# Optimization experiments

Measured on AMD Instinct MI355X. Metric: run time of the kernel, lower is better.

Reference implementation:

```python
import jax, jax.numpy as jnp
import numpy as np

B, H, W = 8, 448, 448
NUM_CLASSES, NUM_FEATURES = 80, 1280
TOPN, THRESHOLD = 4, 0.5


def conv(x, w, b, stride, pad):
    y = jax.lax.conv_general_dilated(x, w, (stride, stride), [(pad, pad), (pad, pad)],
                                     dimension_numbers=('NCHW', 'OIHW', 'NCHW'))
    return y + b[None, :, None, None]


def sample_bilinear(img, ys, xs):
    # img: [C, Hs, Ws]; ys: [oh] float coords; xs: [ow] float coords (align_corners=True grid)
    Hs, Ws = img.shape[1], img.shape[2]
    y0 = jnp.clip(jnp.floor(ys), 0.0, Hs - 1.0)
    x0 = jnp.clip(jnp.floor(xs), 0.0, Ws - 1.0)
    y0i = y0.astype(jnp.int32); y1i = jnp.minimum(y0i + 1, Hs - 1)
    x0i = x0.astype(jnp.int32); x1i = jnp.minimum(x0i + 1, Ws - 1)
    wy = (ys - y0)[:, None]   # [oh,1]
    wx = (xs - x0)[None, :]   # [1,ow]
    r0 = img[:, y0i, :]; r1 = img[:, y1i, :]          # [C,oh,Ws]
    a = r0[:, :, x0i]; b_ = r0[:, :, x1i]             # [C,oh,ow]
    c = r1[:, :, x0i]; d = r1[:, :, x1i]
    top = a * (1.0 - wx) + b_ * wx
    bot = c * (1.0 - wx) + d * wx
    return top * (1.0 - wy) + bot * wy


def minmax_norm(s):
    # torch: if max==min: s/max else (s-min)/(max-min); sigmoid output so max>0
    mn = s.min(-1, keepdims=True); mx = s.max(-1, keepdims=True)
    rng = mx - mn
    return jnp.where(rng > 0, (s - mn) / jnp.where(rng > 0, rng, 1.0),
                     s / jnp.where(mx != 0, mx, 1.0))


def obj_loc(score, threshold, dim):
    # first/last threshold crossing with min-size fallback (vectorized over leading dims)
    mask = score >= threshold
    any_ = mask.any(-1)
    first = jnp.argmax(mask, axis=-1)
    last = dim - jnp.argmax(mask[..., ::-1], axis=-1)   # exclusive
    lo = jnp.where(any_, first, int(dim * 0.125)).astype(jnp.int32)
    hi = jnp.where(any_, last, int(dim * 0.875)).astype(jnp.int32)
    minsize = int(np.ceil(dim * 0.125))
    need = jnp.maximum(minsize - (hi - lo), 0)
    lo = jnp.maximum(lo - (need + 1) // 2, 0)
    hi = jnp.minimum(hi + (need + 1) // 2, dim)
    return lo, hi


def one_crop(img, y1, y2, x1, x2):
    # crop img[:, y1:y2, x1:x2] and bilinearly resize to (H,W), align_corners=True
    oh, ow = img.shape[1], img.shape[2]
    ys = y1.astype(jnp.float32) + jnp.arange(oh, dtype=jnp.float32) * ((y2 - 1 - y1).astype(jnp.float32) / (oh - 1))
    xs = x1.astype(jnp.float32) + jnp.arange(ow, dtype=jnp.float32) * ((x2 - 1 - x1).astype(jnp.float32) / (ow - 1))
    return sample_bilinear(img, ys, xs)


def setup_inputs() -> dict:
    key = jax.random.key(0)
    k1, k2, k3 = jax.random.split(key, 3)
    return {
        'inputs': jax.random.normal(k1, (B, 3, H, W), dtype=jnp.float32),
        'feat_w': jax.random.normal(k2, (NUM_FEATURES, 3, 3, 3), dtype=jnp.float32) * 0.05,
        'feat_b': jnp.zeros((NUM_FEATURES,), dtype=jnp.float32),
        'cls_w': jax.random.normal(k3, (NUM_CLASSES, NUM_FEATURES, 1, 1), dtype=jnp.float32) * 0.02,
        'cls_b': jnp.zeros((NUM_CLASSES,), dtype=jnp.float32),
    }


def reference(inputs, feat_w, feat_b, cls_w, cls_b):
    b, c, h, w = inputs.shape
    # ---- backbone (stride-32 stand-in for MobileNetV2 features) ----
    ga = jnp.clip(conv(inputs, feat_w, feat_b, 32, 1), 0.0, 6.0)     # [b,1280,h/32,w/32]
    gf = ga.mean((2, 3), keepdims=True)                               # avg pool sh=h/32
    gs = jax.nn.sigmoid(conv(gf, cls_w, cls_b, 1, 0)).reshape(b, -1)  # [b,num_classes]
    # ---- CAM score path (on detached ga) ----
    cam = jax.nn.sigmoid(conv(jax.lax.stop_gradient(ga), cls_w, cls_b, 1, 0))
    ys_g = jnp.linspace(0.0, cam.shape[2] - 1.0, h)
    xs_g = jnp.linspace(0.0, cam.shape[3] - 1.0, w)
    cam_up = jax.vmap(lambda im: sample_bilinear(im, ys_g, xs_g))(cam)  # [b,C,h,w]
    wscore = cam_up.max(axis=2)   # max over height -> [b,C,w]
    hscore = cam_up.max(axis=3)   # max over width  -> [b,C,h]
    # ---- topN classes by global score ----
    _, topi = jax.lax.top_k(gs, TOPN)                                  # [b,topN]
    xs_s = jnp.take_along_axis(wscore, topi[:, :, None], axis=1)       # [b,topN,w]
    ys_s = jnp.take_along_axis(hscore, topi[:, :, None], axis=1)       # [b,topN,h]
    x1, x2 = obj_loc(minmax_norm(xs_s), THRESHOLD, w)
    y1, y2 = obj_loc(minmax_norm(ys_s), THRESHOLD, h)
    # ---- dynamic crop + bilinear resize, vectorized over (b, topN) ----
    crops = jax.vmap(lambda img, a1, a2, b1, b2:
                     jax.vmap(lambda p, q, r, s: one_crop(img, p, q, r, s))(a1, a2, b1, b2)
                     )(inputs, y1, y2, x1, x2)                          # [b,topN,3,h,w]
    li = jax.lax.stop_gradient(crops.reshape(b * TOPN, 3, h, w))
    la = jnp.clip(conv(li, feat_w, feat_b, 32, 1), 0.0, 6.0)
    lf = la.mean((2, 3), keepdims=True)
    ls = jax.nn.sigmoid(conv(lf, cls_w, cls_b, 1, 0)).reshape(b, TOPN, -1).max(axis=1)
    return gs, ls
```

## Files before the change

### kernel.cpp

```cpp
#include <hip/hip_runtime.h>
#include <math.h>

#define NB 8
#define TOPN 4
#define NC 80
#define NF 1280
#define HW 448
#define OS 14
#define NP 196
#define NPCH 49
#define PATCH (3*42*42)

__device__ __forceinline__ float sigmoidf_(float x) { return 1.0f / (1.0f + expf(-x)); }

__device__ __forceinline__ double wave_reduce_f64(double v) {
#pragma unroll
  for (int off = 32; off > 0; off >>= 1) v += __shfl_down(v, off);
  return v;
}

__global__ __launch_bounds__(256) void k1_conv_global(
    const float* __restrict__ in,
    const float* __restrict__ fw,
    const float* __restrict__ fb,
    float* __restrict__ ga,
    double* __restrict__ gfp)
{
  __shared__ float patch[PATCH];
  const int b = blockIdx.y, fc = blockIdx.x, pz = blockIdx.z, tid = threadIdx.x;
  for (int i = tid; i < PATCH; i += 256) {
    int c = i / 1764, rem = i % 1764, r = rem / 42, cc = rem % 42;
    int row = 32 * (r / 3) + (r % 3) - 1;
    int col = 32 * (cc / 3) + (cc % 3) - 1;
    float v = 0.0f;
    if (row >= 0 && col >= 0)
      v = in[((b * 3 + c) * HW + row) * HW + col];
    patch[i] = v;
  }
  __syncthreads();
  const int f = fc * 256 + tid;
  float w[27];
#pragma unroll
  for (int k = 0; k < 27; ++k) w[k] = fw[f * 27 + k];
  const float bias = fb[f];
  double sum = 0.0;
#pragma unroll 7
  for (int pi = 0; pi < NPCH; ++pi) {
    const int p = pz * NPCH + pi;
    const int oy = p / OS, ox = p % OS;
    float acc = bias;
#pragma unroll
    for (int c = 0; c < 3; ++c)
#pragma unroll
      for (int ky = 0; ky < 3; ++ky)
#pragma unroll
        for (int kx = 0; kx < 3; ++kx)
          acc += patch[c * 1764 + (oy * 3 + ky) * 42 + (ox * 3 + kx)] * w[c * 9 + ky * 3 + kx];
    acc = fminf(fmaxf(acc, 0.0f), 6.0f);
    ga[((size_t)b * NP + p) * NF + f] = acc;
    sum += (double)acc;
  }
  gfp[((size_t)pz * NB + b) * NF + f] = sum;
}

__global__ __launch_bounds__(64) void k2a_gs(
    const double* __restrict__ gfp,
    const float* __restrict__ cw,
    const float* __restrict__ cb,
    float* __restrict__ gs_out)
{
  const int cls = blockIdx.x, b = blockIdx.y, lane = threadIdx.x;
  const float* w = cw + (size_t)cls * NF;
  const double* g0 = gfp + ((size_t)0 * NB + b) * NF;
  const double* g1 = gfp + ((size_t)1 * NB + b) * NF;
  const double* g2 = gfp + ((size_t)2 * NB + b) * NF;
  const double* g3 = gfp + ((size_t)3 * NB + b) * NF;
  double acc = 0.0;
#pragma unroll
  for (int k = 0; k < NF / 64; ++k) {
    const int f = k * 64 + lane;
    const double gv = (double)(float)((g0[f] + g1[f] + g2[f] + g3[f]) / 196.0);
    acc += (double)w[f] * gv;
  }
  acc = wave_reduce_f64(acc);
  if (lane == 0) gs_out[b * NC + cls] = sigmoidf_((float)(acc + (double)cb[cls]));
}

__global__ __launch_bounds__(64) void k2b_topk(
    const float* __restrict__ gs,
    int* __restrict__ topi)
{
  const int b = blockIdx.x, lane = threadIdx.x;
  float v0 = gs[b * NC + lane];
  float v1 = (lane < NC - 64) ? gs[b * NC + 64 + lane] : -1e30f;
  const int i0 = lane, i1 = 64 + lane;
#pragma unroll
  for (int t = 0; t < TOPN; ++t) {
    float bv; int bi;
    if (v1 > v0) { bv = v1; bi = i1; } else { bv = v0; bi = i0; }
#pragma unroll
    for (int off = 1; off < 64; off <<= 1) {
      float ov = __shfl_xor(bv, off);
      int oi = __shfl_xor(bi, off);
      if (ov > bv || (ov == bv && oi < bi)) { bv = ov; bi = oi; }
    }
    if (lane == 0) topi[b * TOPN + t] = bi;
    if (bi == i0) v0 = -1e30f;
    if (bi == i1) v1 = -1e30f;
  }
}

__global__ __launch_bounds__(256) void k3a_cam(
    const float* __restrict__ ga,
    const float* __restrict__ cw,
    const float* __restrict__ cb,
    const int* __restrict__ topi,
    float* __restrict__ camg)
{
  const int pc = blockIdx.x, bt = blockIdx.y;
  const int tid = threadIdx.x, wid = tid >> 6, lane = tid & 63;
  const int p = pc * 4 + wid;
  const int b = bt >> 2;
  const int cls = topi[bt];
  const float* w = cw + (size_t)cls * NF;
  const float* g = ga + ((size_t)b * NP + p) * NF;
  double acc = 0.0;
#pragma unroll
  for (int k = 0; k < NF / 64; ++k) {
    const int f = k * 64 + lane;
    acc += (double)g[f] * (double)w[f];
  }
  acc = wave_reduce_f64(acc);
  if (lane == 0) camg[bt * NP + p] = sigmoidf_((float)(acc + (double)cb[cls]));
}

__global__ __launch_bounds__(256) void k3b_bounds_stage(
    const float* __restrict__ camg,
    const float* __restrict__ in,
    float* __restrict__ patchg)
{
  __shared__ float cam[NP];
  __shared__ float wsS[HW];
  __shared__ float hsS[HW];
  __shared__ int jlo[OS], jhi[OS];
  __shared__ int shb[4];
  const int bt = blockIdx.x, tid = threadIdx.x;
  const int wid = tid >> 6, lane = tid & 63;
  const float SC = 13.0f / 447.0f;

  if (tid < OS) { jlo[tid] = 1 << 30; jhi[tid] = -1; }
  for (int i = tid; i < NP; i += 256) cam[i] = camg[bt * NP + i];
  __syncthreads();
  for (int j = tid; j < HW; j += 256) {
    float yp = (float)j * SC;
    int y0 = (int)floorf(yp); if (y0 > 13) y0 = 13;
    atomicMin(&jlo[y0], j);
    atomicMax(&jhi[y0], j);
  }
  __syncthreads();

  for (int x = tid; x < HW; x += 256) {
    float xp = (float)x * SC;
    int x0 = (int)floorf(xp); if (x0 > 13) x0 = 13;
    float wx = xp - (float)x0;
    int x1i = min(x0 + 1, 13);
    {
      float cv[OS];
#pragma unroll
      for (int r = 0; r < OS; ++r)
        cv[r] = cam[r * OS + x0] * (1.0f - wx) + cam[r * OS + x1i] * wx;
      float m = -1e30f;
#pragma unroll
      for (int r = 0; r < OS; ++r) {
        int jl = jlo[r], jh = jhi[r];
        if (jl <= jh) {
          const int rn = (r + 1 < OS) ? r + 1 : OS - 1;
          float yp1 = (float)jl * SC; float wy1 = yp1 - (float)r;
          float yp2 = (float)jh * SC; float wy2 = yp2 - (float)r;
          float v1 = cv[r] * (1.0f - wy1) + cv[rn] * wy1;
          float v2 = cv[r] * (1.0f - wy2) + cv[rn] * wy2;
          m = fmaxf(m, fmaxf(v1, v2));
        }
      }
      wsS[x] = m;
    }
    {
      float cv[OS];
#pragma unroll
      for (int c = 0; c < OS; ++c)
        cv[c] = cam[x0 * OS + c] * (1.0f - wx) + cam[x1i * OS + c] * wx;
      float m = -1e30f;
#pragma unroll
      for (int r = 0; r < OS; ++r) {
        int jl = jlo[r], jh = jhi[r];
        if (jl <= jh) {
          const int rn = (r + 1 < OS) ? r + 1 : OS - 1;
          float xp1 = (float)jl * SC; float w1 = xp1 - (float)r;
          float xp2 = (float)jh * SC; float w2 = xp2 - (float)r;
          float v1 = cv[r] * (1.0f - w1) + cv[rn] * w1;
          float v2 = cv[r] * (1.0f - w2) + cv[rn] * w2;
          m = fmaxf(m, fmaxf(v1, v2));
        }
      }
      hsS[x] = m;
    }
  }
  __syncthreads();

  if (wid < 2) {
    const float* s = (wid == 0) ? wsS : hsS;
    float v[7];
    float mn = 1e30f, mx = -1e30f;
#pragma unroll
    for (int q = 0; q < 7; ++q) {
      v[q] = s[lane + 64 * q];
      mn = fminf(mn, v[q]); mx = fmaxf(mx, v[q]);
    }
#pragma unroll
    for (int off = 32; off > 0; off >>= 1) {
      mn = fminf(mn, __shfl_down(mn, off));
      mx = fmaxf(mx, __shfl_down(mx, off));
    }
    mn = __shfl(mn, 0); mx = __shfl(mx, 0);
    float rng = mx - mn;
    float dnm = (mx != 0.0f) ? mx : 1.0f;
    int firstL = 1 << 30, lastL = -1;
#pragma unroll
    for (int q = 0; q < 7; ++q) {
      float nv = (rng > 0.0f) ? (v[q] - mn) / rng : v[q] / dnm;
      if (nv >= 0.5f) {
        int idx = lane + 64 * q;
        firstL = min(firstL, idx);
        lastL = max(lastL, idx);
      }
    }
#pragma unroll
    for (int off = 32; off > 0; off >>= 1) {
      firstL = min(firstL, __shfl_down(firstL, off));
      lastL = max(lastL, __shfl_down(lastL, off));
    }
    if (lane == 0) {
      int lo, hi;
      if (lastL >= 0) { lo = firstL; hi = lastL + 1; }
      else { lo = 56; hi = 392; }
      int need = 56 - (hi - lo); if (need < 0) need = 0;
      int pad = (need + 1) >> 1;
      lo = lo - pad; if (lo < 0) lo = 0;
      hi = hi + pad; if (hi > HW) hi = HW;
      if (wid == 0) { shb[2] = lo; shb[3] = hi; }
      else          { shb[0] = lo; shb[1] = hi; }
    }
  }
  __syncthreads();

  const int b = bt >> 2;
  const int y1 = shb[0], y2 = shb[1], x1 = shb[2], x2 = shb[3];
  const float y1f = (float)y1, x1f = (float)x1;
  const float sy = (float)(y2 - 1 - y1) / 447.0f;
  const float sx = (float)(x2 - 1 - x1) / 447.0f;
  const float* img = in + (size_t)b * 3 * HW * HW;
  for (int i = tid; i < PATCH; i += 256) {
    int c = i / 1764, rem = i % 1764, r = rem / 42, cc = rem % 42;
    int yy = 32 * (r / 3) + (r % 3) - 1;
    int xx = 32 * (cc / 3) + (cc % 3) - 1;
    float v = 0.0f;
    if (yy >= 0 && xx >= 0) {
      float ys = y1f + (float)yy * sy;
      float xs = x1f + (float)xx * sx;
      float y0 = floorf(ys); if (y0 < 0.0f) y0 = 0.0f; if (y0 > 447.0f) y0 = 447.0f;
      float x0 = floorf(xs); if (x0 < 0.0f) x0 = 0.0f; if (x0 > 447.0f) x0 = 447.0f;
      int y0i = (int)y0, x0i = (int)x0;
      int y1i = min(y0i + 1, HW - 1), x1i = min(x0i + 1, HW - 1);
      float wy = ys - y0, wx = xs - x0;
      const float* ic = img + (size_t)c * HW * HW;
      float a  = ic[y0i * HW + x0i], bb = ic[y0i * HW + x1i];
      float cc2 = ic[y1i * HW + x0i], d  = ic[y1i * HW + x1i];
      float top = a * (1.0f - wx) + bb * wx;
      float bot = cc2 * (1.0f - wx) + d * wx;
      v = top * (1.0f - wy) + bot * wy;
    }
    patchg[(size_t)bt * PATCH + i] = v;
  }
}

__global__ __launch_bounds__(256) void k4_conv_local(
    const float* __restrict__ patchg,
    const float* __restrict__ fw,
    const float* __restrict__ fb,
    double* __restrict__ lfp)
{
  __shared__ float patch[PATCH];
  const int bt = blockIdx.y, fc = blockIdx.x, pz = blockIdx.z, tid = threadIdx.x;
  for (int i = tid; i < PATCH; i += 256)
    patch[i] = patchg[(size_t)bt * PATCH + i];
  __syncthreads();
  const int f = fc * 256 + tid;
  float w[27];
#pragma unroll
  for (int k = 0; k < 27; ++k) w[k] = fw[f * 27 + k];
  const float bias = fb[f];
  double sum = 0.0;
#pragma unroll 7
  for (int pi = 0; pi < NPCH; ++pi) {
    const int p = pz * NPCH + pi;
    const int oy = p / OS, ox = p % OS;
    float acc = bias;
#pragma unroll
    for (int c = 0; c < 3; ++c)
#pragma unroll
      for (int ky = 0; ky < 3; ++ky)
#pragma unroll
        for (int kx = 0; kx < 3; ++kx)
          acc += patch[c * 1764 + (oy * 3 + ky) * 42 + (ox * 3 + kx)] * w[c * 9 + ky * 3 + kx];
    acc = fminf(fmaxf(acc, 0.0f), 6.0f);
    sum += (double)acc;
  }
  lfp[((size_t)pz * (NB * TOPN) + bt) * NF + f] = sum;
}

__global__ __launch_bounds__(256) void kcomb_lf(
    const double* __restrict__ lfp,
    float* __restrict__ lf32)
{
  const int j = blockIdx.x * 256 + threadIdx.x;
  const double s = lfp[j] + lfp[40960 + j] + lfp[81920 + j] + lfp[122880 + j];
  lf32[j] = (float)(s / 196.0);
}

__global__ __launch_bounds__(64) void k5_ls(
    const float* __restrict__ lf32,
    const float* __restrict__ cw,
    const float* __restrict__ cb,
    float* __restrict__ ls_out)
{
  const int cls = blockIdx.x, b = blockIdx.y, lane = threadIdx.x;
  const float* w = cw + (size_t)cls * NF;
  const float* l0 = lf32 + (size_t)(b * TOPN + 0) * NF;
  const float* l1 = lf32 + (size_t)(b * TOPN + 1) * NF;
  const float* l2 = lf32 + (size_t)(b * TOPN + 2) * NF;
  const float* l3 = lf32 + (size_t)(b * TOPN + 3) * NF;
  double a0 = 0.0, a1 = 0.0, a2 = 0.0, a3 = 0.0;
#pragma unroll
  for (int k = 0; k < NF / 64; ++k) {
    const int f = k * 64 + lane;
    const double wv = (double)w[f];
    a0 += wv * (double)l0[f];
    a1 += wv * (double)l1[f];
    a2 += wv * (double)l2[f];
    a3 += wv * (double)l3[f];
  }
  a0 = wave_reduce_f64(a0);
  a1 = wave_reduce_f64(a1);
  a2 = wave_reduce_f64(a2);
  a3 = wave_reduce_f64(a3);
  if (lane == 0) {
    const double bias = (double)cb[cls];
    float m = sigmoidf_((float)(a0 + bias));
    m = fmaxf(m, sigmoidf_((float)(a1 + bias)));
    m = fmaxf(m, sigmoidf_((float)(a2 + bias)));
    m = fmaxf(m, sigmoidf_((float)(a3 + bias)));
    ls_out[b * NC + cls] = m;
  }
}

extern "C" void kernel_launch(void* const* d_in, const int* in_sizes, int n_in,
                              void* d_out, int out_size, void* d_ws, size_t ws_size,
                              hipStream_t stream) {
  const float* in = (const float*)d_in[0];
  const float* fw = (const float*)d_in[1];
  const float* fb = (const float*)d_in[2];
  const float* cw = (const float*)d_in[3];
  const float* cb = (const float*)d_in[4];
  float* out = (float*)d_out;

  double* gfp = (double*)d_ws;
  double* lfp = gfp + (size_t)4 * NB * NF;
  float* ga = (float*)(lfp + (size_t)4 * NB * TOPN * NF);
  float* lf32 = ga + (size_t)NB * NP * NF;
  float* patchg = lf32 + (size_t)NB * TOPN * NF;
  float* camg = patchg + (size_t)NB * TOPN * PATCH;
  int* topi = (int*)(camg + NB * TOPN * NP);

  k1_conv_global<<<dim3(5, NB, 4), 256, 0, stream>>>(in, fw, fb, ga, gfp);
  k2a_gs<<<dim3(NC, NB), 64, 0, stream>>>(gfp, cw, cb, out);
  k2b_topk<<<NB, 64, 0, stream>>>(out, topi);
  k3a_cam<<<dim3(NPCH, NB * TOPN), 256, 0, stream>>>(ga, cw, cb, topi, camg);
  k3b_bounds_stage<<<NB * TOPN, 256, 0, stream>>>(camg, in, patchg);
  k4_conv_local<<<dim3(5, NB * TOPN, 4), 256, 0, stream>>>(patchg, fw, fb, lfp);
  kcomb_lf<<<NB * TOPN * NF / 256, 256, 0, stream>>>(lfp, lf32);
  k5_ls<<<dim3(NC, NB), 64, 0, stream>>>(lf32, cw, cb, out + 640);
}
```

Measured before the change: 165.6 us.

## Split conv kernels per output row, stage weights in LDS, fuse gs+topk

The global and local conv kernels now run one block per output row (14 z-slices instead of 4), staging only a 3-row input strip and the block's filter weights in LDS. This raises block count for occupancy and makes the weight loads coalesced. The global-score and top-k kernels are fused into a single 1024-thread block per batch, and the CAM kernel caches the class weight row in LDS. The cost is more partial-sum buffers to combine (14 instead of 4) and redundant weight staging per block.

```diff
diff --git a/kernel.cpp b/kernel.cpp
--- a/kernel.cpp
+++ b/kernel.cpp
@@ -8,8 +8,9 @@
 #define HW 448
 #define OS 14
 #define NP 196
-#define NPCH 49
 #define PATCH (3*42*42)
+#define ROWPATCH (3*3*42)
+#define WLDS (256*27)
 
 __device__ __forceinline__ float sigmoidf_(float x) { return 1.0f / (1.0f + expf(-x)); }
 
@@ -26,11 +27,13 @@
     float* __restrict__ ga,
     double* __restrict__ gfp)
 {
-  __shared__ float patch[PATCH];
-  const int b = blockIdx.y, fc = blockIdx.x, pz = blockIdx.z, tid = threadIdx.x;
-  for (int i = tid; i < PATCH; i += 256) {
-    int c = i / 1764, rem = i % 1764, r = rem / 42, cc = rem % 42;
-    int row = 32 * (r / 3) + (r % 3) - 1;
+  __shared__ float patch[ROWPATCH];
+  __shared__ float wlds[WLDS];
+  const int b = blockIdx.y, fc = blockIdx.x, oy = blockIdx.z, tid = threadIdx.x;
+  for (int i = tid; i < WLDS; i += 256) wlds[i] = fw[fc * WLDS + i];
+  for (int i = tid; i < ROWPATCH; i += 256) {
+    int c = i / 126, rem = i % 126, rr = rem / 42, cc = rem % 42;
+    int row = 32 * oy + rr - 1;
     int col = 32 * (cc / 3) + (cc % 3) - 1;
     float v = 0.0f;
     if (row >= 0 && col >= 0)
@@ -41,13 +44,11 @@
   const int f = fc * 256 + tid;
   float w[27];
 #pragma unroll
-  for (int k = 0; k < 27; ++k) w[k] = fw[f * 27 + k];
+  for (int k = 0; k < 27; ++k) w[k] = wlds[tid * 27 + k];
   const float bias = fb[f];
   double sum = 0.0;
 #pragma unroll 7
-  for (int pi = 0; pi < NPCH; ++pi) {
-    const int p = pz * NPCH + pi;
-    const int oy = p / OS, ox = p % OS;
+  for (int ox = 0; ox < OS; ++ox) {
     float acc = bias;
 #pragma unroll
     for (int c = 0; c < 3; ++c)
@@ -55,58 +56,67 @@
       for (int ky = 0; ky < 3; ++ky)
 #pragma unroll
         for (int kx = 0; kx < 3; ++kx)
-          acc += patch[c * 1764 + (oy * 3 + ky) * 42 + (ox * 3 + kx)] * w[c * 9 + ky * 3 + kx];
+          acc += patch[c * 126 + ky * 42 + ox * 3 + kx] * w[c * 9 + ky * 3 + kx];
     acc = fminf(fmaxf(acc, 0.0f), 6.0f);
-    ga[((size_t)b * NP + p) * NF + f] = acc;
+    ga[((size_t)b * NP + oy * OS + ox) * NF + f] = acc;
     sum += (double)acc;
   }
-  gfp[((size_t)pz * NB + b) * NF + f] = sum;
-}
-
-__global__ __launch_bounds__(64) void k2a_gs(
+  gfp[((size_t)oy * NB + b) * NF + f] = sum;
+}
+
+__global__ __launch_bounds__(1024) void k2_gs_topk(
     const double* __restrict__ gfp,
     const float* __restrict__ cw,
     const float* __restrict__ cb,
-    float* __restrict__ gs_out)
-{
-  const int cls = blockIdx.x, b = blockIdx.y, lane = threadIdx.x;
-  const float* w = cw + (size_t)cls * NF;
-  const double* g0 = gfp + ((size_t)0 * NB + b) * NF;
-  const double* g1 = gfp + ((size_t)1 * NB + b) * NF;
-  const double* g2 = gfp + ((size_t)2 * NB + b) * NF;
-  const double* g3 = gfp + ((size_t)3 * NB + b) * NF;
-  double acc = 0.0;
-#pragma unroll
-  for (int k = 0; k < NF / 64; ++k) {
-    const int f = k * 64 + lane;
-    const double gv = (double)(float)((g0[f] + g1[f] + g2[f] + g3[f]) / 196.0);
-    acc += (double)w[f] * gv;
-  }
-  acc = wave_reduce_f64(acc);
-  if (lane == 0) gs_out[b * NC + cls] = sigmoidf_((float)(acc + (double)cb[cls]));
-}
-
-__global__ __launch_bounds__(64) void k2b_topk(
-    const float* __restrict__ gs,
+    float* __restrict__ gs_out,
     int* __restrict__ topi)
 {
-  const int b = blockIdx.x, lane = threadIdx.x;
-  float v0 = gs[b * NC + lane];
-  float v1 = (lane < NC - 64) ? gs[b * NC + 64 + lane] : -1e30f;
-  const int i0 = lane, i1 = 64 + lane;
-#pragma unroll
-  for (int t = 0; t < TOPN; ++t) {
-    float bv; int bi;
-    if (v1 > v0) { bv = v1; bi = i1; } else { bv = v0; bi = i0; }
-#pragma unroll
-    for (int off = 1; off < 64; off <<= 1) {
-      float ov = __shfl_xor(bv, off);
-      int oi = __shfl_xor(bi, off);
-      if (ov > bv || (ov == bv && oi < bi)) { bv = ov; bi = oi; }
-    }
-    if (lane == 0) topi[b * TOPN + t] = bi;
-    if (bi == i0) v0 = -1e30f;
-    if (bi == i1) v1 = -1e30f;
+  __shared__ float gfs[NF];
+  __shared__ float gsv[NC];
+  const int b = blockIdx.x, tid = threadIdx.x;
+  for (int i = tid; i < NF; i += 1024) {
+    double s = 0.0;
+#pragma unroll
+    for (int z = 0; z < OS; ++z) s += gfp[((size_t)z * NB + b) * NF + i];
+    gfs[i] = (float)(s / 196.0);
+  }
+  __syncthreads();
+  const int wid = tid >> 6, lane = tid & 63;
+  for (int j = 0; j < 5; ++j) {
+    const int cls = wid * 5 + j;
+    const float* w = cw + (size_t)cls * NF;
+    double acc = 0.0;
+#pragma unroll
+    for (int k = 0; k < NF / 64; ++k) {
+      int f = k * 64 + lane;
+      acc += (double)w[f] * (double)gfs[f];
+    }
+    acc = wave_reduce_f64(acc);
+    if (lane == 0) {
+      float s = sigmoidf_((float)(acc + (double)cb[cls]));
+      gsv[cls] = s;
+      gs_out[b * NC + cls] = s;
+    }
+  }
+  __syncthreads();
+  if (wid == 0) {
+    float v0 = gsv[lane];
+    float v1 = (lane < NC - 64) ? gsv[64 + lane] : -1e30f;
+    const int i0 = lane, i1 = 64 + lane;
+#pragma unroll
+    for (int t = 0; t < TOPN; ++t) {
+      float bv; int bi;
+      if (v1 > v0) { bv = v1; bi = i1; } else { bv = v0; bi = i0; }
+#pragma unroll
+      for (int off = 1; off < 64; off <<= 1) {
+        float ov = __shfl_xor(bv, off);
+        int oi = __shfl_xor(bi, off);
+        if (ov > bv || (ov == bv && oi < bi)) { bv = ov; bi = oi; }
+      }
+      if (lane == 0) topi[b * TOPN + t] = bi;
+      if (bi == i0) v0 = -1e30f;
+      if (bi == i1) v1 = -1e30f;
+    }
   }
 }
 
@@ -117,18 +127,20 @@
     const int* __restrict__ topi,
     float* __restrict__ camg)
 {
+  __shared__ float clsw[NF];
   const int pc = blockIdx.x, bt = blockIdx.y;
   const int tid = threadIdx.x, wid = tid >> 6, lane = tid & 63;
   const int p = pc * 4 + wid;
   const int b = bt >> 2;
   const int cls = topi[bt];
-  const float* w = cw + (size_t)cls * NF;
+  for (int i = tid; i < NF; i += 256) clsw[i] = cw[(size_t)cls * NF + i];
+  __syncthreads();
   const float* g = ga + ((size_t)b * NP + p) * NF;
   double acc = 0.0;
 #pragma unroll
   for (int k = 0; k < NF / 64; ++k) {
     const int f = k * 64 + lane;
-    acc += (double)g[f] * (double)w[f];
+    acc += (double)g[f] * (double)clsw[f];
   }
   acc = wave_reduce_f64(acc);
   if (lane == 0) camg[bt * NP + p] = sigmoidf_((float)(acc + (double)cb[cls]));
@@ -289,21 +301,23 @@
     const float* __restrict__ fb,
     double* __restrict__ lfp)
 {
-  __shared__ float patch[PATCH];
-  const int bt = blockIdx.y, fc = blockIdx.x, pz = blockIdx.z, tid = threadIdx.x;
-  for (int i = tid; i < PATCH; i += 256)
-    patch[i] = patchg[(size_t)bt * PATCH + i];
+  __shared__ float patch[ROWPATCH];
+  __shared__ float wlds[WLDS];
+  const int bt = blockIdx.y, fc = blockIdx.x, oy = blockIdx.z, tid = threadIdx.x;
+  for (int i = tid; i < WLDS; i += 256) wlds[i] = fw[fc * WLDS + i];
+  for (int i = tid; i < ROWPATCH; i += 256) {
+    int c = i / 126, rem = i % 126, rr = rem / 42, cc = rem % 42;
+    patch[i] = patchg[(size_t)bt * PATCH + c * 1764 + (3 * oy + rr) * 42 + cc];
+  }
   __syncthreads();
   const int f = fc * 256 + tid;
   float w[27];
 #pragma unroll
-  for (int k = 0; k < 27; ++k) w[k] = fw[f * 27 + k];
+  for (int k = 0; k < 27; ++k) w[k] = wlds[tid * 27 + k];
   const float bias = fb[f];
   double sum = 0.0;
 #pragma unroll 7
-  for (int pi = 0; pi < NPCH; ++pi) {
-    const int p = pz * NPCH + pi;
-    const int oy = p / OS, ox = p % OS;
+  for (int ox = 0; ox < OS; ++ox) {
     float acc = bias;
 #pragma unroll
     for (int c = 0; c < 3; ++c)
@@ -311,11 +325,11 @@
       for (int ky = 0; ky < 3; ++ky)
 #pragma unroll
         for (int kx = 0; kx < 3; ++kx)
-          acc += patch[c * 1764 + (oy * 3 + ky) * 42 + (ox * 3 + kx)] * w[c * 9 + ky * 3 + kx];
+          acc += patch[c * 126 + ky * 42 + ox * 3 + kx] * w[c * 9 + ky * 3 + kx];
     acc = fminf(fmaxf(acc, 0.0f), 6.0f);
     sum += (double)acc;
   }
-  lfp[((size_t)pz * (NB * TOPN) + bt) * NF + f] = sum;
+  lfp[((size_t)oy * (NB * TOPN) + bt) * NF + f] = sum;
 }
 
 __global__ __launch_bounds__(256) void kcomb_lf(
@@ -323,7 +337,9 @@
     float* __restrict__ lf32)
 {
   const int j = blockIdx.x * 256 + threadIdx.x;
-  const double s = lfp[j] + lfp[40960 + j] + lfp[81920 + j] + lfp[122880 + j];
+  double s = 0.0;
+#pragma unroll
+  for (int z = 0; z < OS; ++z) s += lfp[(size_t)z * 40960 + j];
   lf32[j] = (float)(s / 196.0);
 }
 
@@ -374,19 +390,18 @@
   float* out = (float*)d_out;
 
   double* gfp = (double*)d_ws;
-  double* lfp = gfp + (size_t)4 * NB * NF;
-  float* ga = (float*)(lfp + (size_t)4 * NB * TOPN * NF);
+  double* lfp = gfp + (size_t)OS * NB * NF;
+  float* ga = (float*)(lfp + (size_t)OS * NB * TOPN * NF);
   float* lf32 = ga + (size_t)NB * NP * NF;
   float* patchg = lf32 + (size_t)NB * TOPN * NF;
   float* camg = patchg + (size_t)NB * TOPN * PATCH;
   int* topi = (int*)(camg + NB * TOPN * NP);
 
-  k1_conv_global<<<dim3(5, NB, 4), 256, 0, stream>>>(in, fw, fb, ga, gfp);
-  k2a_gs<<<dim3(NC, NB), 64, 0, stream>>>(gfp, cw, cb, out);
-  k2b_topk<<<NB, 64, 0, stream>>>(out, topi);
-  k3a_cam<<<dim3(NPCH, NB * TOPN), 256, 0, stream>>>(ga, cw, cb, topi, camg);
+  k1_conv_global<<<dim3(5, NB, OS), 256, 0, stream>>>(in, fw, fb, ga, gfp);
+  k2_gs_topk<<<NB, 1024, 0, stream>>>(gfp, cw, cb, out, topi);
+  k3a_cam<<<dim3(NP / 4, NB * TOPN), 256, 0, stream>>>(ga, cw, cb, topi, camg);
   k3b_bounds_stage<<<NB * TOPN, 256, 0, stream>>>(camg, in, patchg);
-  k4_conv_local<<<dim3(5, NB * TOPN, 4), 256, 0, stream>>>(patchg, fw, fb, lfp);
+  k4_conv_local<<<dim3(5, NB * TOPN, OS), 256, 0, stream>>>(patchg, fw, fb, lfp);
   kcomb_lf<<<NB * TOPN * NF / 256, 256, 0, stream>>>(lfp, lf32);
   k5_ls<<<dim3(NC, NB), 64, 0, stream>>>(lf32, cw, cb, out + 640);
 }
```

After: 144.6 us, median of 2. -12.6%, faster.
